# Optimization experiments

Measured on AMD Instinct MI355X. Metric: run time of the kernel, lower is better.

The kernel has to match this reference:

```python
import jax, jax.numpy as jnp
import numpy as np

B = 256; NROIS = 200; IN = 200; HID = 128; L = 4; H = 8; RATIO = 0.5
K = int(np.ceil(RATIO * NROIS))        # SAGPooling top-k per graph = 100
N = B * NROIS                          # total nodes = 51200
DEG = 32; EPG = NROIS * DEG; E_EDGES = B * EPG  # 1,638,400 edges
EMB = HID * L                          # MHA embed dim = 512
DH = EMB // H

def _xavier(k, shape):
    fan_in, fan_out = shape[-2], shape[-1]
    lim = float(np.sqrt(6.0 / (fan_in + fan_out)))
    return jax.random.uniform(k, shape, jnp.float32, -lim, lim)

def setup_inputs() -> dict:
    key = jax.random.key(0)
    ks = jax.random.split(key, 16)
    x = jax.random.normal(ks[0], (N, IN), jnp.float32)
    # block-diagonal edge list: edges stay within each graph's node range
    src = jax.random.randint(ks[1], (E_EDGES,), 0, NROIS, jnp.int32)
    dst = jax.random.randint(ks[2], (E_EDGES,), 0, NROIS, jnp.int32)
    off = jnp.repeat(jnp.arange(B, dtype=jnp.int32) * NROIS, EPG)
    edge_index = jnp.stack([src + off, dst + off])
    edge_attr = jax.random.normal(ks[3], (E_EDGES,), jnp.float32)  # unused by the math
    batch = jnp.repeat(jnp.arange(B, dtype=jnp.int32), NROIS)
    return dict(
        x=x, edge_index=edge_index, edge_attr=edge_attr, batch=batch,
        gcn_w0=_xavier(ks[4], (IN, HID)),
        gcn_w=_xavier(ks[5], (L - 1, HID, HID)),
        gcn_b=jnp.zeros((L, HID), jnp.float32),
        lin1_w0=_xavier(ks[6], (IN + HID, HID)),
        lin1_w=_xavier(ks[7], (L - 1, 2 * HID, HID)),
        lin1_b=jnp.zeros((L, HID), jnp.float32),
        lin2_w=_xavier(ks[8], (L, HID, HID)),
        lin2_b=jnp.zeros((L, HID), jnp.float32),
        sag_w1=_xavier(ks[9], (HID, 1)),
        sag_w2=_xavier(ks[10], (HID, 1)),
        sag_b=jnp.zeros((1,), jnp.float32),
        mha_in_w=_xavier(ks[11], (3 * EMB, EMB)),
        mha_in_b=jnp.zeros((3 * EMB,), jnp.float32),
        mha_out_w=_xavier(ks[12], (EMB, EMB)),
        mha_out_b=jnp.zeros((EMB,), jnp.float32),
        fin_w=_xavier(ks[13], (EMB, HID)),
        fin_b=jnp.zeros((HID,), jnp.float32),
    )

def _gcn_conv(x, src, dst, W, b):
    xw = x @ W
    deg = jax.ops.segment_sum(jnp.ones_like(dst, jnp.float32), dst, num_segments=N) + 1.0
    dinv = jax.lax.rsqrt(deg)
    norm = dinv[src] * dinv[dst]                     # [E]
    agg = jax.ops.segment_sum(xw[src] * norm[:, None], dst, num_segments=N)
    agg = agg + xw * (dinv * dinv)[:, None]          # self-loop term
    return agg + b

def _gcblock(x, src, dst, gw, gb, l1w, l1b, l2w, l2b):
    x1 = jnp.tanh(_gcn_conv(x, src, dst, gw, gb))
    h = jnp.tanh(jnp.concatenate([x, x1], axis=1) @ l1w + l1b)
    return jnp.tanh(h @ l2w + l2b)

def _sag_pool_pad(z, src, dst, w1, w2, b):
    # SAGPooling score via PyG GraphConv (aggr='add'): lin_rel(sum_j x_j) + lin_root(x_i)
    neigh = jax.ops.segment_sum(z[src], dst, num_segments=N)
    score = (neigh @ w1)[:, 0] + b[0] + (z @ w2)[:, 0]        # [N]
    s3 = score.reshape(B, NROIS)
    vals, idx = jax.lax.top_k(s3, K)                           # [B,K]
    z3 = z.reshape(B, NROIS, HID)
    pooled = jnp.take_along_axis(z3, idx[:, :, None], axis=1) * jnp.tanh(vals)[:, :, None]
    zpad = jnp.zeros_like(z3).at[jnp.arange(B)[:, None], idx].set(pooled)
    return zpad.reshape(N, HID)

def reference(x, edge_index, edge_attr, batch,
              gcn_w0, gcn_w, gcn_b, lin1_w0, lin1_w, lin1_b, lin2_w, lin2_b,
              sag_w1, sag_w2, sag_b,
              mha_in_w, mha_in_b, mha_out_w, mha_out_b, fin_w, fin_b):
    src, dst = edge_index[0], edge_index[1]
    z = x
    pads = []
    for i in range(L):
        gw = gcn_w0 if i == 0 else gcn_w[i - 1]
        l1w = lin1_w0 if i == 0 else lin1_w[i - 1]
        z = _gcblock(z, src, dst, gw, gcn_b[i], l1w, lin1_b[i], lin2_w[i], lin2_b[i])
        pads.append(_sag_pool_pad(z, src, dst, sag_w1, sag_w2, sag_b))
    xc = jnp.concatenate(pads, axis=1).reshape(B, NROIS, EMB)   # [B,S,E]
    # MultiheadAttention (batch_first, eval mode -> no dropout)
    qkv = xc @ mha_in_w.T + mha_in_b                             # [B,S,3E]
    q, k, v = jnp.split(qkv, 3, axis=-1)
    def heads(t):
        return t.reshape(B, NROIS, H, DH).transpose(0, 2, 1, 3)  # [B,H,S,dh]
    q, k, v = heads(q), heads(k), heads(v)
    scores = jnp.einsum('bhqd,bhkd->bhqk', q, k) / np.sqrt(DH)
    attn = jax.nn.softmax(scores, axis=-1)                       # [B,H,S,S]
    o = jnp.einsum('bhqk,bhkd->bhqd', attn, v).transpose(0, 2, 1, 3).reshape(B, NROIS, EMB)
    o = o @ mha_out_w.T + mha_out_b
    attn_weights = attn.mean(axis=1)                             # avg over heads [B,S,S]
    # readout: global_mean_pool over each graph's nrois nodes
    pooled = o.mean(axis=1)                                      # [B,E]
    out = jnp.tanh(pooled @ fin_w + fin_b)                       # [B,HID]
    return out, attn_weights
```

## Files before the change

kernel.cpp:

```cpp
#include <hip/hip_runtime.h>
#include <hip/hip_fp16.h>


#define GB   256
#define SS   200
#define KIN  200
#define HD   128
#define NLAY 4
#define NHD  8
#define TOPK 100
#define NT   (GB * SS)
#define EPG_ 6400
#define NE_  (GB * EPG_)
#define EMB_ 512

typedef _Float16 half8 __attribute__((ext_vector_type(8)));
typedef _Float16 half4v __attribute__((ext_vector_type(4)));
typedef float floatx4 __attribute__((ext_vector_type(4)));

__global__ __launch_bounds__(256) void k_build_A(const int* __restrict__ src,
                                                 const int* __restrict__ dst,
                                                 float* __restrict__ A) {
  int e = blockIdx.x * 256 + threadIdx.x;
  if (e >= NE_) return;
  int d = dst[e], s = src[e];
  int b = d / SS;
  int dl = d - b * SS;
  int sl = s - b * SS;
  atomicAdd(&A[((size_t)b * SS + dl) * SS + sl], 1.0f);
}

__global__ __launch_bounds__(256) void k_dinv(const float* __restrict__ A,
                                              float* __restrict__ dinv) {
  int node = blockIdx.x * 4 + (threadIdx.x >> 6);
  int lane = threadIdx.x & 63;
  const float* r = A + (size_t)node * SS;
  float v = r[lane] + r[lane + 64] + r[lane + 128];
  if (lane < 8) v += r[lane + 192];
#pragma unroll
  for (int o = 32; o; o >>= 1) v += __shfl_xor(v, o);
  if (lane == 0) dinv[node] = rsqrtf(v + 1.0f);
}

__global__ __launch_bounds__(256) void k_prep_all(
    const float* __restrict__ gcn_w0, const float* __restrict__ gcn_w,
    const float* __restrict__ lin1_w0, const float* __restrict__ lin1_w,
    const float* __restrict__ lin2_w,
    __half* __restrict__ whi, __half* __restrict__ wlo) {
  const int mat = blockIdx.x >> 7;
  const int n   = blockIdx.x & 127;
  const int l = mat / 3, which = mat % 3;
  const float* src;
  int K, Kpad;
  if (which == 0) {
    K = l ? HD : KIN;  Kpad = l ? 128 : 256;
    src = l ? gcn_w + (size_t)(l - 1) * HD * HD : gcn_w0;
  } else if (which == 1) {
    K = l ? 2 * HD : KIN + HD;  Kpad = l ? 256 : 384;
    src = l ? lin1_w + (size_t)(l - 1) * 2 * HD * HD : lin1_w0;
  } else {
    K = HD;  Kpad = HD;
    src = lin2_w + (size_t)l * HD * HD;
  }
  int off = (l == 0) ? (which == 0 ? 0 : (which == 1 ? 32768 : 81920))
                     : 98304 + (l - 1) * 65536 +
                       (which == 0 ? 0 : (which == 1 ? 16384 : 49152));
  _Float16* wh = (_Float16*)whi + (size_t)off + (size_t)n * Kpad;
  _Float16* wl = (_Float16*)wlo + (size_t)off + (size_t)n * Kpad;
  for (int k = threadIdx.x; k < Kpad; k += 256) {
    float v = (k < K) ? src[(size_t)k * HD + n] : 0.f;
    _Float16 h = (_Float16)v;
    wh[k] = h;
    wl[k] = (_Float16)(v - (float)h);
  }
}

__global__ __launch_bounds__(256) void k_prep_w16(const float* __restrict__ W,
                                                  __half* __restrict__ W16) {
  int i = blockIdx.x * 256 + threadIdx.x;
  float4 v = reinterpret_cast<const float4*>(W)[i];
  half4v h = {(_Float16)v.x, (_Float16)v.y, (_Float16)v.z, (_Float16)v.w};
  *reinterpret_cast<half4v*>((_Float16*)W16 + (size_t)i * 4) = h;
}

__global__ __launch_bounds__(256) void k_node_mfma(
    const float* __restrict__ in1, int k1,
    const float* __restrict__ in2,
    const __half* __restrict__ Whi, const __half* __restrict__ Wlo,
    int Kpad,
    const float* __restrict__ bias,
    float* __restrict__ out, int doTanh) {
  const int m0 = blockIdx.x * 64;
  const int t = threadIdx.x;
  const int wave = t >> 6, lane = t & 63;
  const int col = lane & 15, quad = lane >> 4;
  const int wm = (wave & 1) * 32;
  const int wn = (wave >> 1) * 64;
  __shared__ __align__(16) _Float16 Ah[64][72];
  __shared__ __align__(16) _Float16 Al[64][72];
  floatx4 acc[2][4] = {};
  const int lr = t >> 2;
  const int lk = (t & 3) * 16;
  const _Float16* Wh = (const _Float16*)Whi;
  const _Float16* Wl = (const _Float16*)Wlo;

  for (int k0 = 0; k0 < Kpad; k0 += 64) {
    __syncthreads();
#pragma unroll
    for (int q = 0; q < 4; ++q) {
      int kg = k0 + lk + q * 4;
      float4 v = {0.f, 0.f, 0.f, 0.f};
      if (kg < k1)
        v = *reinterpret_cast<const float4*>(&in1[(size_t)(m0 + lr) * k1 + kg]);
      else if (in2 && kg < k1 + HD)
        v = *reinterpret_cast<const float4*>(&in2[(size_t)(m0 + lr) * HD + (kg - k1)]);
      half4v h = {(_Float16)v.x, (_Float16)v.y, (_Float16)v.z, (_Float16)v.w};
      half4v lo = {(_Float16)(v.x - (float)h.x), (_Float16)(v.y - (float)h.y),
                   (_Float16)(v.z - (float)h.z), (_Float16)(v.w - (float)h.w)};
      *reinterpret_cast<half4v*>(&Ah[lr][lk + q * 4]) = h;
      *reinterpret_cast<half4v*>(&Al[lr][lk + q * 4]) = lo;
    }
    __syncthreads();
#pragma unroll
    for (int ks = 0; ks < 2; ++ks) {
      half8 ah[2], al[2], bh[4], bl[4];
#pragma unroll
      for (int i = 0; i < 2; ++i) {
        ah[i] = *reinterpret_cast<const half8*>(&Ah[wm + i * 16 + col][ks * 32 + quad * 8]);
        al[i] = *reinterpret_cast<const half8*>(&Al[wm + i * 16 + col][ks * 32 + quad * 8]);
      }
#pragma unroll
      for (int j = 0; j < 4; ++j) {
        const size_t wo = (size_t)(wn + j * 16 + col) * Kpad + k0 + ks * 32 + quad * 8;
        bh[j] = *reinterpret_cast<const half8*>(Wh + wo);
        bl[j] = *reinterpret_cast<const half8*>(Wl + wo);
      }
#pragma unroll
      for (int i = 0; i < 2; ++i)
#pragma unroll
        for (int j = 0; j < 4; ++j) {
          acc[i][j] = __builtin_amdgcn_mfma_f32_16x16x32_f16(ah[i], bh[j], acc[i][j], 0, 0, 0);
          acc[i][j] = __builtin_amdgcn_mfma_f32_16x16x32_f16(ah[i], bl[j], acc[i][j], 0, 0, 0);
          acc[i][j] = __builtin_amdgcn_mfma_f32_16x16x32_f16(al[i], bh[j], acc[i][j], 0, 0, 0);
        }
    }
  }
#pragma unroll
  for (int j = 0; j < 4; ++j) {
    int n = wn + j * 16 + col;
    float bb = bias ? bias[n] : 0.f;
#pragma unroll
    for (int i = 0; i < 2; ++i) {
      int rbase = m0 + wm + i * 16 + quad * 4;
#pragma unroll
      for (int r = 0; r < 4; ++r) {
        float v = acc[i][j][r] + bb;
        if (doTanh) v = tanhf(v);
        out[(size_t)(rbase + r) * HD + n] = v;
      }
    }
  }
}

__global__ __launch_bounds__(256) void k_fused(
    const float* __restrict__ in1, int k1,
    const float* __restrict__ x1,
    const __half* __restrict__ l1wh, const __half* __restrict__ l1wl, int KP1,
    const float* __restrict__ l1b,
    const __half* __restrict__ l2wh, const __half* __restrict__ l2wl,
    const float* __restrict__ l2b,
    const __half* __restrict__ gwh, const __half* __restrict__ gwl,
    float* __restrict__ zout, float* __restrict__ xwout) {
  const int m0 = blockIdx.x * 64;
  const int t = threadIdx.x;
  const int wave = t >> 6, lane = t & 63;
  const int col = lane & 15, quad = lane >> 4;
  const int wm = (wave & 1) * 32;
  const int wn = (wave >> 1) * 64;
  __shared__ __align__(16) _Float16 Ah[64][72];
  __shared__ __align__(16) _Float16 Al[64][72];
  __shared__ __align__(16) _Float16 Hh[64][136];
  __shared__ __align__(16) _Float16 Hl[64][136];
  const int lr = t >> 2;
  const int lk = (t & 3) * 16;

  {
    floatx4 acc[2][4] = {};
    for (int k0 = 0; k0 < KP1; k0 += 64) {
      __syncthreads();
#pragma unroll
      for (int q = 0; q < 4; ++q) {
        int kg = k0 + lk + q * 4;
        float4 v = {0.f, 0.f, 0.f, 0.f};
        if (kg < k1)
          v = *reinterpret_cast<const float4*>(&in1[(size_t)(m0 + lr) * k1 + kg]);
        else if (kg < k1 + HD)
          v = *reinterpret_cast<const float4*>(&x1[(size_t)(m0 + lr) * HD + (kg - k1)]);
        half4v h = {(_Float16)v.x, (_Float16)v.y, (_Float16)v.z, (_Float16)v.w};
        half4v lo = {(_Float16)(v.x - (float)h.x), (_Float16)(v.y - (float)h.y),
                     (_Float16)(v.z - (float)h.z), (_Float16)(v.w - (float)h.w)};
        *reinterpret_cast<half4v*>(&Ah[lr][lk + q * 4]) = h;
        *reinterpret_cast<half4v*>(&Al[lr][lk + q * 4]) = lo;
      }
      __syncthreads();
#pragma unroll
      for (int ks = 0; ks < 2; ++ks) {
        half8 ah[2], al[2], bh[4], bl[4];
#pragma unroll
        for (int i = 0; i < 2; ++i) {
          ah[i] = *reinterpret_cast<const half8*>(&Ah[wm + i * 16 + col][ks * 32 + quad * 8]);
          al[i] = *reinterpret_cast<const half8*>(&Al[wm + i * 16 + col][ks * 32 + quad * 8]);
        }
#pragma unroll
        for (int j = 0; j < 4; ++j) {
          const size_t wo = (size_t)(wn + j * 16 + col) * KP1 + k0 + ks * 32 + quad * 8;
          bh[j] = *reinterpret_cast<const half8*>((const _Float16*)l1wh + wo);
          bl[j] = *reinterpret_cast<const half8*>((const _Float16*)l1wl + wo);
        }
#pragma unroll
        for (int i = 0; i < 2; ++i)
#pragma unroll
          for (int j = 0; j < 4; ++j) {
            acc[i][j] = __builtin_amdgcn_mfma_f32_16x16x32_f16(ah[i], bh[j], acc[i][j], 0, 0, 0);
            acc[i][j] = __builtin_amdgcn_mfma_f32_16x16x32_f16(ah[i], bl[j], acc[i][j], 0, 0, 0);
            acc[i][j] = __builtin_amdgcn_mfma_f32_16x16x32_f16(al[i], bh[j], acc[i][j], 0, 0, 0);
          }
      }
    }
#pragma unroll
    for (int j = 0; j < 4; ++j) {
      int n = wn + j * 16 + col;
      float bb = l1b[n];
#pragma unroll
      for (int i = 0; i < 2; ++i) {
        int rb = wm + i * 16 + quad * 4;
#pragma unroll
        for (int r = 0; r < 4; ++r) {
          float v = tanhf(acc[i][j][r] + bb);
          _Float16 h = (_Float16)v;
          Hh[rb + r][n] = h;
          Hl[rb + r][n] = (_Float16)(v - (float)h);
        }
      }
    }
  }
  __syncthreads();

  {
    floatx4 acc[2][4] = {};
#pragma unroll
    for (int kc = 0; kc < 4; ++kc) {
      half8 ah[2], al[2], bh[4], bl[4];
#pragma unroll
      for (int i = 0; i < 2; ++i) {
        ah[i] = *reinterpret_cast<const half8*>(&Hh[wm + i * 16 + col][kc * 32 + quad * 8]);
        al[i] = *reinterpret_cast<const half8*>(&Hl[wm + i * 16 + col][kc * 32 + quad * 8]);
      }
#pragma unroll
      for (int j = 0; j < 4; ++j) {
        const size_t wo = (size_t)(wn + j * 16 + col) * HD + kc * 32 + quad * 8;
        bh[j] = *reinterpret_cast<const half8*>((const _Float16*)l2wh + wo);
        bl[j] = *reinterpret_cast<const half8*>((const _Float16*)l2wl + wo);
      }
#pragma unroll
      for (int i = 0; i < 2; ++i)
#pragma unroll
        for (int j = 0; j < 4; ++j) {
          acc[i][j] = __builtin_amdgcn_mfma_f32_16x16x32_f16(ah[i], bh[j], acc[i][j], 0, 0, 0);
          acc[i][j] = __builtin_amdgcn_mfma_f32_16x16x32_f16(ah[i], bl[j], acc[i][j], 0, 0, 0);
          acc[i][j] = __builtin_amdgcn_mfma_f32_16x16x32_f16(al[i], bh[j], acc[i][j], 0, 0, 0);
        }
    }
    __syncthreads();
#pragma unroll
    for (int j = 0; j < 4; ++j) {
      int n = wn + j * 16 + col;
      float bb = l2b[n];
#pragma unroll
      for (int i = 0; i < 2; ++i) {
        int rb = wm + i * 16 + quad * 4;
#pragma unroll
        for (int r = 0; r < 4; ++r) {
          float v = tanhf(acc[i][j][r] + bb);
          zout[(size_t)(m0 + rb + r) * HD + n] = v;
          _Float16 h = (_Float16)v;
          Hh[rb + r][n] = h;
          Hl[rb + r][n] = (_Float16)(v - (float)h);
        }
      }
    }
  }
  if (!gwh) return;
  __syncthreads();

  {
    floatx4 acc[2][4] = {};
#pragma unroll
    for (int kc = 0; kc < 4; ++kc) {
      half8 ah[2], al[2], bh[4], bl[4];
#pragma unroll
      for (int i = 0; i < 2; ++i) {
        ah[i] = *reinterpret_cast<const half8*>(&Hh[wm + i * 16 + col][kc * 32 + quad * 8]);
        al[i] = *reinterpret_cast<const half8*>(&Hl[wm + i * 16 + col][kc * 32 + quad * 8]);
      }
#pragma unroll
      for (int j = 0; j < 4; ++j) {
        const size_t wo = (size_t)(wn + j * 16 + col) * HD + kc * 32 + quad * 8;
        bh[j] = *reinterpret_cast<const half8*>((const _Float16*)gwh + wo);
        bl[j] = *reinterpret_cast<const half8*>((const _Float16*)gwl + wo);
      }
#pragma unroll
      for (int i = 0; i < 2; ++i)
#pragma unroll
        for (int j = 0; j < 4; ++j) {
          acc[i][j] = __builtin_amdgcn_mfma_f32_16x16x32_f16(ah[i], bh[j], acc[i][j], 0, 0, 0);
          acc[i][j] = __builtin_amdgcn_mfma_f32_16x16x32_f16(ah[i], bl[j], acc[i][j], 0, 0, 0);
          acc[i][j] = __builtin_amdgcn_mfma_f32_16x16x32_f16(al[i], bh[j], acc[i][j], 0, 0, 0);
        }
    }
#pragma unroll
    for (int j = 0; j < 4; ++j) {
      int n = wn + j * 16 + col;
#pragma unroll
      for (int i = 0; i < 2; ++i) {
        int rb = wm + i * 16 + quad * 4;
#pragma unroll
        for (int r = 0; r < 4; ++r)
          xwout[(size_t)(m0 + rb + r) * HD + n] = acc[i][j][r];
      }
    }
  }
}

__global__ __launch_bounds__(256) void k_agg_mfma(
    const float* __restrict__ A, const float* __restrict__ dinv,
    const float* __restrict__ xw, const float* __restrict__ bias,
    float* __restrict__ out) {
  const int b    = blockIdx.x >> 1;
  const int row0 = (blockIdx.x & 1) * 128;
  const int t = threadIdx.x;
  const int wave = t >> 6, lane = t & 63;
  const int col = lane & 15, quad = lane >> 4;
  const int wm = (wave & 1) * 64, wn = (wave >> 1) * 64;
  __shared__ __align__(16) _Float16 Ah[128][72];
  __shared__ __align__(16) _Float16 Al[128][72];
  __shared__ __align__(16) _Float16 Bh[128][72];
  __shared__ __align__(16) _Float16 Bl[128][72];
  __shared__ float dvs[256];
  dvs[t] = (t < SS) ? dinv[b * SS + t] : 0.f;
  floatx4 acc[4][4] = {};
  const float* Ab  = A  + (size_t)b * SS * SS;
  const float* xwb = xw + (size_t)b * SS * HD;
  const int lr = t >> 1, lk = (t & 1) * 32;
  const int d = row0 + lr;
  __syncthreads();
  const float dvd = (d < SS) ? dvs[d] : 0.f;

  for (int k0 = 0; k0 < 256; k0 += 64) {
    __syncthreads();
#pragma unroll
    for (int q = 0; q < 8; ++q) {
      int s = k0 + lk + q * 4;
      float4 v = {0.f, 0.f, 0.f, 0.f};
      if (d < SS && s < SS)
        v = *reinterpret_cast<const float4*>(&Ab[(size_t)d * SS + s]);
      float e0 = (v.x + ((s + 0 == d) ? 1.f : 0.f)) * dvd * dvs[(s + 0) & 255];
      float e1 = (v.y + ((s + 1 == d) ? 1.f : 0.f)) * dvd * dvs[(s + 1) & 255];
      float e2 = (v.z + ((s + 2 == d) ? 1.f : 0.f)) * dvd * dvs[(s + 2) & 255];
      float e3 = (v.w + ((s + 3 == d) ? 1.f : 0.f)) * dvd * dvs[(s + 3) & 255];
      half4v h = {(_Float16)e0, (_Float16)e1, (_Float16)e2, (_Float16)e3};
      half4v lo = {(_Float16)(e0 - (float)h.x), (_Float16)(e1 - (float)h.y),
                   (_Float16)(e2 - (float)h.z), (_Float16)(e3 - (float)h.w)};
      *reinterpret_cast<half4v*>(&Ah[lr][lk + q * 4]) = h;
      *reinterpret_cast<half4v*>(&Al[lr][lk + q * 4]) = lo;
    }
#pragma unroll
    for (int p = 0; p < 8; ++p) {
      int idx = t + p * 256;
      int c4 = idx & 31, ss = idx >> 5;
      int s = k0 + ss;
      float4 v = {0.f, 0.f, 0.f, 0.f};
      if (s < SS)
        v = *reinterpret_cast<const float4*>(&xwb[(size_t)s * HD + c4 * 4]);
      int ssx = ss ^ ((c4 & 7) << 3);
      float e[4] = {v.x, v.y, v.z, v.w};
#pragma unroll
      for (int j = 0; j < 4; ++j) {
        _Float16 h = (_Float16)e[j];
        Bh[c4 * 4 + j][ssx] = h;
        Bl[c4 * 4 + j][ssx] = (_Float16)(e[j] - (float)h);
      }
    }
    __syncthreads();
#pragma unroll
    for (int ks = 0; ks < 2; ++ks) {
      half8 ah[4], al[4], bh[4], bl[4];
#pragma unroll
      for (int i = 0; i < 4; ++i) {
        ah[i] = *reinterpret_cast<const half8*>(&Ah[wm + i * 16 + col][ks * 32 + quad * 8]);
        al[i] = *reinterpret_cast<const half8*>(&Al[wm + i * 16 + col][ks * 32 + quad * 8]);
      }
#pragma unroll
      for (int j = 0; j < 4; ++j) {
        int n = wn + j * 16 + col;
        int koff = (ks * 32 + quad * 8) ^ (((n >> 2) & 7) << 3);
        bh[j] = *reinterpret_cast<const half8*>(&Bh[n][koff]);
        bl[j] = *reinterpret_cast<const half8*>(&Bl[n][koff]);
      }
#pragma unroll
      for (int i = 0; i < 4; ++i)
#pragma unroll
        for (int j = 0; j < 4; ++j) {
          acc[i][j] = __builtin_amdgcn_mfma_f32_16x16x32_f16(ah[i], bh[j], acc[i][j], 0, 0, 0);
          acc[i][j] = __builtin_amdgcn_mfma_f32_16x16x32_f16(ah[i], bl[j], acc[i][j], 0, 0, 0);
          acc[i][j] = __builtin_amdgcn_mfma_f32_16x16x32_f16(al[i], bh[j], acc[i][j], 0, 0, 0);
        }
    }
  }
#pragma unroll
  for (int j = 0; j < 4; ++j) {
    int n = wn + j * 16 + col;
    float bb = bias[n];
#pragma unroll
    for (int i = 0; i < 4; ++i) {
      int rbase = row0 + wm + i * 16 + quad * 4;
#pragma unroll
      for (int r = 0; r < 4; ++r) {
        int row = rbase + r;
        if (row < SS)
          out[((size_t)b * SS + row) * HD + n] = tanhf(acc[i][j][r] + bb);
      }
    }
  }
}

__global__ __launch_bounds__(256) void k_sag(
    const float* __restrict__ z, const float* __restrict__ A,
    const float* __restrict__ w1, const float* __restrict__ w2,
    const float* __restrict__ sb,
    __half* __restrict__ xch, __half* __restrict__ xcl, int layer) {
  const int b = blockIdx.x, t = threadIdx.x;
  __shared__ float w1s[HD], w2s[HD];
  __shared__ float zw1[SS], sc[SS], fac[SS];
  if (t < HD) { w1s[t] = w1[t]; w2s[t] = w2[t]; }
  __syncthreads();
  float a2 = 0.f;
  if (t < SS) {
    const float4* zr = reinterpret_cast<const float4*>(&z[((size_t)b * SS + t) * HD]);
    float a1 = 0.f;
#pragma unroll
    for (int q = 0; q < HD / 4; ++q) {
      float4 v = zr[q];
      a1 += v.x * w1s[4 * q] + v.y * w1s[4 * q + 1] + v.z * w1s[4 * q + 2] + v.w * w1s[4 * q + 3];
      a2 += v.x * w2s[4 * q] + v.y * w2s[4 * q + 1] + v.z * w2s[4 * q + 2] + v.w * w2s[4 * q + 3];
    }
    zw1[t] = a1;
  }
  __syncthreads();
  if (t < SS) {
    float s = sb[0] + a2;
    const float4* ar = reinterpret_cast<const float4*>(&A[((size_t)b * SS + t) * SS]);
#pragma unroll 5
    for (int q = 0; q < SS / 4; ++q) {
      float4 v = ar[q];
      s += v.x * zw1[4 * q] + v.y * zw1[4 * q + 1] + v.z * zw1[4 * q + 2] + v.w * zw1[4 * q + 3];
    }
    sc[t] = s;
  }
  __syncthreads();
  if (t < SS) {
    float si = sc[t];
    int cnt = 0;
    for (int j = 0; j < SS; ++j) {
      float sj = sc[j];
      cnt += (sj > si || (sj == si && j < t)) ? 1 : 0;
    }
    fac[t] = (cnt < TOPK) ? tanhf(si) : 0.f;
  }
  __syncthreads();
  _Float16* xh = (_Float16*)xch;
  _Float16* xl = (_Float16*)xcl;
  for (int idx = t; idx < SS * HD; idx += 256) {
    int row = idx >> 7, c = idx & 127;
    float v = fac[row] * z[((size_t)b * SS + row) * HD + c];
    _Float16 h = (_Float16)v;
    size_t o = ((size_t)b * SS + row) * EMB_ + layer * HD + c;
    xh[o] = h;
    xl[o] = (_Float16)(v - (float)h);
  }
}

__global__ __launch_bounds__(256) void k_proj(
    const __half* __restrict__ xch, const __half* __restrict__ Win16,
    const float* __restrict__ bin, __half* __restrict__ QKh) {
  const int wg = (blockIdx.x & 7) * 400 + (blockIdx.x >> 3);
  const int bm = wg >> 3;
  const int bn = wg & 7;
  const int m0 = bm * 128, n0 = bn * 128;
  const int t = threadIdx.x;
  const int wave = t >> 6, lane = t & 63;
  const int col = lane & 15, quad = lane >> 4;
  const int wm = (wave & 1) * 64;
  const int wn = (wave >> 1) * 64;
  __shared__ __align__(16) _Float16 As[128][64];
  __shared__ __align__(16) _Float16 Bs[128][64];
  floatx4 acc[4][4] = {};
  const _Float16* X = (const _Float16*)xch;
  const _Float16* W = (const _Float16*)Win16;

  const int srow = lane >> 3;
  const int sch  = (lane & 7) ^ srow;
  const int arow = wave * 8 + srow;
  const int fsw = col & 7;

  for (int k0 = 0; k0 < EMB_; k0 += 64) {
#pragma unroll
    for (int q = 0; q < 4; ++q) {
      const _Float16* ga = X + (size_t)(m0 + q * 32 + arow) * EMB_ + k0 + sch * 8;
      __builtin_amdgcn_global_load_lds(
          (const __attribute__((address_space(1))) void*)ga,
          (__attribute__((address_space(3))) void*)((char*)&As[0][0] + q * 4096 + wave * 1024),
          16, 0, 0);
      const _Float16* gb = W + (size_t)(n0 + q * 32 + arow) * EMB_ + k0 + sch * 8;
      __builtin_amdgcn_global_load_lds(
          (const __attribute__((address_space(1))) void*)gb,
          (__attribute__((address_space(3))) void*)((char*)&Bs[0][0] + q * 4096 + wave * 1024),
          16, 0, 0);
    }
    __syncthreads();
#pragma unroll
    for (int ks = 0; ks < 2; ++ks) {
      const int ch = (ks * 4 + quad) ^ fsw;
      half8 af[4], bf[4];
#pragma unroll
      for (int i = 0; i < 4; ++i)
        af[i] = *reinterpret_cast<const half8*>(
            (const char*)&As[0][0] + (wm + i * 16 + col) * 128 + ch * 16);
#pragma unroll
      for (int j = 0; j < 4; ++j)
        bf[j] = *reinterpret_cast<const half8*>(
            (const char*)&Bs[0][0] + (wn + j * 16 + col) * 128 + ch * 16);
#pragma unroll
      for (int i = 0; i < 4; ++i)
#pragma unroll
        for (int j = 0; j < 4; ++j)
          acc[i][j] = __builtin_amdgcn_mfma_f32_16x16x32_f16(af[i], bf[j], acc[i][j], 0, 0, 0);
    }
    __syncthreads();
  }
#pragma unroll
  for (int j = 0; j < 4; ++j) {
    int c = n0 + wn + j * 16 + col;
    float bb = bin[c];
#pragma unroll
    for (int i = 0; i < 4; ++i) {
      int rbase = m0 + wm + i * 16 + quad * 4;
#pragma unroll
      for (int r = 0; r < 4; ++r)
        QKh[(size_t)(rbase + r) * 1024 + c] = __float2half(acc[i][j][r] + bb);
    }
  }
}

__global__ __launch_bounds__(256) void k_attn(
    const __half* __restrict__ QKh,
    float* __restrict__ cpbuf,
    float* __restrict__ attn) {
  const int bx = (blockIdx.x & 7) * 416 + (blockIdx.x >> 3);
  const int b  = bx / 13;
  const int it = bx % 13;
  const int i0 = it * 16;
  const int rows = (SS - i0 >= 16) ? 16 : (SS - i0);
  const int t    = threadIdx.x;
  const int wave = t >> 6;
  const int lane = t & 63;
  const int col  = lane & 15;
  const int quad = lane >> 4;

  __shared__ __align__(16) float Ss[16][212];

  float am[13];
  int   soff[13];
  int   kmax = 0;
#pragma unroll
  for (int k = 0; k < 13; ++k) {
    int idx = t + (k << 8);
    am[k] = 0.f;
    if (idx < rows * 200) {
      int i = idx / 200;
      soff[k] = idx + 12 * i;
      kmax = k + 1;
    } else soff[k] = 0;
  }

  const _Float16* Qbase = (const _Float16*)QKh + (size_t)b * SS * 1024;
  const _Float16* qrow = Qbase + (size_t)(i0 + col) * 1024 + quad * 8;
  const _Float16* krow[4];
#pragma unroll
  for (int m = 0; m < 4; ++m) {
    int jt = wave + m * 4;
    krow[m] = Qbase + (size_t)(jt * 16 + col) * 1024 + 512 + quad * 8;
  }

  for (int h = 0; h < NHD; ++h) {
    const int hoff = h * 64;
    half8 a0 = *reinterpret_cast<const half8*>(qrow + hoff);
    half8 a1 = *reinterpret_cast<const half8*>(qrow + hoff + 32);
#pragma unroll
    for (int m = 0; m < 4; ++m) {
      int jt = wave + m * 4;
      if (jt < 13) {
        half8 b0 = *reinterpret_cast<const half8*>(krow[m] + hoff);
        half8 b1 = *reinterpret_cast<const half8*>(krow[m] + hoff + 32);
        floatx4 acc = {0.f, 0.f, 0.f, 0.f};
        acc = __builtin_amdgcn_mfma_f32_16x16x32_f16(a0, b0, acc, 0, 0, 0);
        acc = __builtin_amdgcn_mfma_f32_16x16x32_f16(a1, b1, acc, 0, 0, 0);
#pragma unroll
        for (int r = 0; r < 4; ++r)
          Ss[quad * 4 + r][jt * 16 + col] = acc[r] * 0.125f;
      }
    }
    __syncthreads();
#pragma unroll
    for (int ri = 0; ri < 4; ++ri) {
      int r = wave * 4 + ri;
      if (r < rows) {
        float* srow = &Ss[r][0];
        float s0 = srow[lane], s1 = srow[lane + 64], s2 = srow[lane + 128];
        float s3 = (lane < 8) ? srow[lane + 192] : -1e30f;
        float mx = fmaxf(fmaxf(s0, s1), fmaxf(s2, s3));
#pragma unroll
        for (int o = 32; o; o >>= 1) mx = fmaxf(mx, __shfl_xor(mx, o));
        float e0 = __expf(s0 - mx), e1 = __expf(s1 - mx), e2 = __expf(s2 - mx);
        float e3 = (lane < 8) ? __expf(s3 - mx) : 0.f;
        float sum = e0 + e1 + e2 + e3;
#pragma unroll
        for (int o = 32; o; o >>= 1) sum += __shfl_xor(sum, o);
        float rl = 1.0f / sum;
        srow[lane] = e0 * rl; srow[lane + 64] = e1 * rl; srow[lane + 128] = e2 * rl;
        if (lane < 8) srow[lane + 192] = e3 * rl;
      }
    }
    __syncthreads();
    const float* sflat = &Ss[0][0];
#pragma unroll
    for (int k = 0; k < 13; ++k)
      if (k < kmax) am[k] += sflat[soff[k]] * 0.125f;
    if (t < SS) {
      float s = 0.f;
      for (int i = 0; i < rows; ++i) s += Ss[i][t];
      atomicAdd(&cpbuf[((size_t)b * NHD + h) * SS + t], s);
    }
    __syncthreads();
  }
  float* abase = &attn[((size_t)b * SS + i0) * SS];
#pragma unroll
  for (int k = 0; k < 13; ++k)
    if (k < kmax) abase[t + (k << 8)] = am[k];
}

__global__ __launch_bounds__(256) void k_pool(
    const __half* __restrict__ xch, const __half* __restrict__ xcl,
    const float* __restrict__ cpbuf,
    const float* __restrict__ Win, const float* __restrict__ bin,
    float* __restrict__ pooled) {
  const int b = blockIdx.x, t = threadIdx.x;
  __shared__ float cps[NHD][SS];
  __shared__ float tvs[NHD][EMB_];
  for (int idx = t; idx < NHD * SS; idx += 256) {
    int h = idx / SS, j = idx - h * SS;
    cps[h][j] = cpbuf[((size_t)b * NHD + h) * SS + j];
  }
  __syncthreads();
  const _Float16* xh = (const _Float16*)xch + (size_t)b * SS * EMB_;
  const _Float16* xl = (const _Float16*)xcl + (size_t)b * SS * EMB_;
  float a0[NHD] = {0.f}, a1[NHD] = {0.f};
  for (int j = 0; j < SS; ++j) {
    float x0 = (float)xh[(size_t)j * EMB_ + t] + (float)xl[(size_t)j * EMB_ + t];
    float x1 = (float)xh[(size_t)j * EMB_ + t + 256] + (float)xl[(size_t)j * EMB_ + t + 256];
#pragma unroll
    for (int h = 0; h < NHD; ++h) {
      float c = cps[h][j];
      a0[h] += c * x0; a1[h] += c * x1;
    }
  }
#pragma unroll
  for (int h = 0; h < NHD; ++h) { tvs[h][t] = a0[h]; tvs[h][t + 256] = a1[h]; }
  __syncthreads();
  const int wv = t >> 6, lane = t & 63;
  for (int e = wv; e < EMB_; e += 4) {
    int h = e >> 6;
    const float* wr = Win + (size_t)(2 * EMB_ + e) * EMB_;
    float s = 0.f;
#pragma unroll
    for (int q = 0; q < 8; ++q) s += wr[lane + q * 64] * tvs[h][lane + q * 64];
#pragma unroll
    for (int o = 32; o; o >>= 1) s += __shfl_xor(s, o);
    if (lane == 0) pooled[(size_t)b * EMB_ + e] = bin[2 * EMB_ + e] * (float)SS + s;
  }
}

__global__ __launch_bounds__(256) void k_final(
    const float* __restrict__ pooled, const float* __restrict__ Wout,
    const float* __restrict__ bout, const float* __restrict__ finw,
    const float* __restrict__ finb, float* __restrict__ out) {
  const int b = blockIdx.x, t = threadIdx.x;
  __shared__ float pl[EMB_], po[EMB_];
  for (int k = t; k < EMB_; k += 256) pl[k] = pooled[(size_t)b * EMB_ + k] * (1.0f / (float)SS);
  __syncthreads();
  for (int e = t; e < EMB_; e += 256) {
    const float* wr = &Wout[(size_t)e * EMB_];
    float a = bout[e];
    for (int k = 0; k < EMB_; ++k) a += wr[k] * pl[k];
    po[e] = a;
  }
  __syncthreads();
  if (t < HD) {
    float a = finb[t];
    for (int e = 0; e < EMB_; ++e) a += po[e] * finw[(size_t)e * HD + t];
    out[(size_t)b * HD + t] = tanhf(a);
  }
}

extern "C" void kernel_launch(void* const* d_in, const int* in_sizes, int n_in,
                              void* d_out, int out_size, void* d_ws, size_t ws_size,
                              hipStream_t stream) {
  const float* x         = (const float*)d_in[0];
  const int*   ei        = (const int*)d_in[1];
  const float* gcn_w0    = (const float*)d_in[4];
  const float* gcn_w     = (const float*)d_in[5];
  const float* gcn_b     = (const float*)d_in[6];
  const float* lin1_w0   = (const float*)d_in[7];
  const float* lin1_w    = (const float*)d_in[8];
  const float* lin1_b    = (const float*)d_in[9];
  const float* lin2_w    = (const float*)d_in[10];
  const float* lin2_b    = (const float*)d_in[11];
  const float* sag_w1    = (const float*)d_in[12];
  const float* sag_w2    = (const float*)d_in[13];
  const float* sag_b     = (const float*)d_in[14];
  const float* mha_in_w  = (const float*)d_in[15];
  const float* mha_in_b  = (const float*)d_in[16];
  const float* mha_out_w = (const float*)d_in[17];
  const float* mha_out_b = (const float*)d_in[18];
  const float* fin_w     = (const float*)d_in[19];
  const float* fin_b     = (const float*)d_in[20];

  float* ws     = (float*)d_ws;
  float* dinv   = ws;
  float* Araw   = dinv + NT;
  float* buf0   = Araw + (size_t)GB * SS * SS;
  float* buf1   = buf0 + (size_t)NT * HD;
  float* zbuf   = buf1 + (size_t)NT * HD;
  float* xcf    = zbuf + (size_t)NT * HD;
  __half* xch   = (__half*)xcf;
  __half* xcl   = xch + (size_t)NT * EMB_;
  float* pooled = xcf + (size_t)NT * EMB_;
  __half* QKh  = (__half*)Araw;
  float* cpbuf = Araw + 26214400;

  float* outp = (float*)d_out;
  float* attn = outp + (size_t)GB * HD;

  __half* whi   = (__half*)attn;
  __half* wlo   = whi + 294912;
  __half* Win16 = wlo + 294912;

  hipMemsetAsync(Araw, 0, (size_t)GB * SS * SS * sizeof(float), stream);

  k_prep_all<<<12 * 128, 256, 0, stream>>>(gcn_w0, gcn_w, lin1_w0, lin1_w, lin2_w, whi, wlo);
  k_prep_w16<<<512, 256, 0, stream>>>(mha_in_w, Win16);
  k_build_A<<<NE_ / 256, 256, 0, stream>>>(ei, ei + NE_, Araw);
  k_dinv<<<NT / 4, 256, 0, stream>>>(Araw, dinv);

  static const int KP1[4]  = {384, 256, 256, 256};
  static const int OFFg[4] = {0, 98304, 163840, 229376};
  static const int OFF1[4] = {32768, 114688, 180224, 245760};
  static const int OFF2[4] = {81920, 147456, 212992, 278528};

  k_node_mfma<<<NT / 64, 256, 0, stream>>>(x, KIN, nullptr,
                                           whi + OFFg[0], wlo + OFFg[0], 256,
                                           nullptr, buf0, 0);

  for (int l = 0; l < NLAY; ++l) {
    const float* zin = (l == 0) ? x : zbuf;
    int k1 = (l == 0) ? KIN : HD;
    k_agg_mfma<<<GB * 2, 256, 0, stream>>>(Araw, dinv, buf0, gcn_b + l * HD, buf1);
    k_fused<<<NT / 64, 256, 0, stream>>>(
        zin, k1, buf1,
        whi + OFF1[l], wlo + OFF1[l], KP1[l], lin1_b + l * HD,
        whi + OFF2[l], wlo + OFF2[l], lin2_b + l * HD,
        (l < NLAY - 1) ? whi + OFFg[l + 1] : (const __half*)nullptr,
        (l < NLAY - 1) ? wlo + OFFg[l + 1] : (const __half*)nullptr,
        zbuf, buf0);
    k_sag<<<GB, 256, 0, stream>>>(zbuf, Araw, sag_w1, sag_w2, sag_b, xch, xcl, l);
  }

  hipMemsetAsync(cpbuf, 0, (size_t)GB * NHD * SS * sizeof(float), stream);
  k_proj<<<(NT / 128) * 8, 256, 0, stream>>>(xch, Win16, mha_in_b, QKh);
  k_attn<<<GB * 13, 256, 0, stream>>>(QKh, cpbuf, attn);
  k_pool<<<GB, 256, 0, stream>>>(xch, xcl, cpbuf, mha_in_w, mha_in_b, pooled);
  k_final<<<GB, 256, 0, stream>>>(pooled, mha_out_w, mha_out_b, fin_w, fin_b, outp);
}
```

Baseline: 1.372 ms.

## Factor GCN normalization out of A, drop A-lo MFMA, retile softmax and SAG dot

In the GCN aggregation, the D^-1/2 scaling moves off the adjacency tile. Source-side scaling goes onto the xw operand and destination-side scaling onto the epilogue, so A+I (small integer counts) fits exactly in fp16. That removes the low-half A buffer and one of three MFMAs per tile. The SAG score loop gets four independent accumulators, and the attention softmax switches from one row per wave to sixteen lanes per row, using shorter shuffles across all 256 threads. The A split is exact only while edge counts stay fp16-representable.

```diff
diff --git a/kernel.cpp b/kernel.cpp
--- a/kernel.cpp
+++ b/kernel.cpp
@@ -343,7 +343,6 @@
   const int col = lane & 15, quad = lane >> 4;
   const int wm = (wave & 1) * 64, wn = (wave >> 1) * 64;
   __shared__ __align__(16) _Float16 Ah[128][72];
-  __shared__ __align__(16) _Float16 Al[128][72];
   __shared__ __align__(16) _Float16 Bh[128][72];
   __shared__ __align__(16) _Float16 Bl[128][72];
   __shared__ float dvs[256];
@@ -354,7 +353,6 @@
   const int lr = t >> 1, lk = (t & 1) * 32;
   const int d = row0 + lr;
   __syncthreads();
-  const float dvd = (d < SS) ? dvs[d] : 0.f;
 
   for (int k0 = 0; k0 < 256; k0 += 64) {
     __syncthreads();
@@ -364,15 +362,12 @@
       float4 v = {0.f, 0.f, 0.f, 0.f};
       if (d < SS && s < SS)
         v = *reinterpret_cast<const float4*>(&Ab[(size_t)d * SS + s]);
-      float e0 = (v.x + ((s + 0 == d) ? 1.f : 0.f)) * dvd * dvs[(s + 0) & 255];
-      float e1 = (v.y + ((s + 1 == d) ? 1.f : 0.f)) * dvd * dvs[(s + 1) & 255];
-      float e2 = (v.z + ((s + 2 == d) ? 1.f : 0.f)) * dvd * dvs[(s + 2) & 255];
-      float e3 = (v.w + ((s + 3 == d) ? 1.f : 0.f)) * dvd * dvs[(s + 3) & 255];
-      half4v h = {(_Float16)e0, (_Float16)e1, (_Float16)e2, (_Float16)e3};
-      half4v lo = {(_Float16)(e0 - (float)h.x), (_Float16)(e1 - (float)h.y),
-                   (_Float16)(e2 - (float)h.z), (_Float16)(e3 - (float)h.w)};
+      if (s + 0 == d) v.x += 1.0f;
+      if (s + 1 == d) v.y += 1.0f;
+      if (s + 2 == d) v.z += 1.0f;
+      if (s + 3 == d) v.w += 1.0f;
+      half4v h = {(_Float16)v.x, (_Float16)v.y, (_Float16)v.z, (_Float16)v.w};
       *reinterpret_cast<half4v*>(&Ah[lr][lk + q * 4]) = h;
-      *reinterpret_cast<half4v*>(&Al[lr][lk + q * 4]) = lo;
     }
 #pragma unroll
     for (int p = 0; p < 8; ++p) {
@@ -382,8 +377,9 @@
       float4 v = {0.f, 0.f, 0.f, 0.f};
       if (s < SS)
         v = *reinterpret_cast<const float4*>(&xwb[(size_t)s * HD + c4 * 4]);
+      float dvv = dvs[s & 255];
       int ssx = ss ^ ((c4 & 7) << 3);
-      float e[4] = {v.x, v.y, v.z, v.w};
+      float e[4] = {v.x * dvv, v.y * dvv, v.z * dvv, v.w * dvv};
 #pragma unroll
       for (int j = 0; j < 4; ++j) {
         _Float16 h = (_Float16)e[j];
@@ -394,12 +390,10 @@
     __syncthreads();
 #pragma unroll
     for (int ks = 0; ks < 2; ++ks) {
-      half8 ah[4], al[4], bh[4], bl[4];
-#pragma unroll
-      for (int i = 0; i < 4; ++i) {
+      half8 ah[4], bh[4], bl[4];
+#pragma unroll
+      for (int i = 0; i < 4; ++i)
         ah[i] = *reinterpret_cast<const half8*>(&Ah[wm + i * 16 + col][ks * 32 + quad * 8]);
-        al[i] = *reinterpret_cast<const half8*>(&Al[wm + i * 16 + col][ks * 32 + quad * 8]);
-      }
 #pragma unroll
       for (int j = 0; j < 4; ++j) {
         int n = wn + j * 16 + col;
@@ -413,7 +407,6 @@
         for (int j = 0; j < 4; ++j) {
           acc[i][j] = __builtin_amdgcn_mfma_f32_16x16x32_f16(ah[i], bh[j], acc[i][j], 0, 0, 0);
           acc[i][j] = __builtin_amdgcn_mfma_f32_16x16x32_f16(ah[i], bl[j], acc[i][j], 0, 0, 0);
-          acc[i][j] = __builtin_amdgcn_mfma_f32_16x16x32_f16(al[i], bh[j], acc[i][j], 0, 0, 0);
         }
     }
   }
@@ -428,7 +421,7 @@
       for (int r = 0; r < 4; ++r) {
         int row = rbase + r;
         if (row < SS)
-          out[((size_t)b * SS + row) * HD + n] = tanhf(acc[i][j][r] + bb);
+          out[((size_t)b * SS + row) * HD + n] = tanhf(dvs[row] * acc[i][j][r] + bb);
       }
     }
   }
@@ -458,14 +451,21 @@
   }
   __syncthreads();
   if (t < SS) {
-    float s = sb[0] + a2;
+    float s0 = 0.f, s1 = 0.f, s2 = 0.f, s3 = 0.f;
     const float4* ar = reinterpret_cast<const float4*>(&A[((size_t)b * SS + t) * SS]);
-#pragma unroll 5
-    for (int q = 0; q < SS / 4; ++q) {
-      float4 v = ar[q];
-      s += v.x * zw1[4 * q] + v.y * zw1[4 * q + 1] + v.z * zw1[4 * q + 2] + v.w * zw1[4 * q + 3];
-    }
-    sc[t] = s;
+#pragma unroll
+    for (int q = 0; q < SS / 4; q += 4) {
+      float4 v0 = ar[q], v1 = ar[q + 1];
+      float4 v2 = (q + 2 < SS / 4) ? ar[q + 2] : float4{0.f, 0.f, 0.f, 0.f};
+      float4 v3 = (q + 3 < SS / 4) ? ar[q + 3] : float4{0.f, 0.f, 0.f, 0.f};
+      s0 += v0.x * zw1[4 * q] + v0.y * zw1[4 * q + 1] + v0.z * zw1[4 * q + 2] + v0.w * zw1[4 * q + 3];
+      s1 += v1.x * zw1[4 * q + 4] + v1.y * zw1[4 * q + 5] + v1.z * zw1[4 * q + 6] + v1.w * zw1[4 * q + 7];
+      if (q + 2 < SS / 4)
+        s2 += v2.x * zw1[4 * q + 8] + v2.y * zw1[4 * q + 9] + v2.z * zw1[4 * q + 10] + v2.w * zw1[4 * q + 11];
+      if (q + 3 < SS / 4)
+        s3 += v3.x * zw1[4 * q + 12] + v3.y * zw1[4 * q + 13] + v3.z * zw1[4 * q + 14] + v3.w * zw1[4 * q + 15];
+    }
+    sc[t] = sb[0] + a2 + ((s0 + s1) + (s2 + s3));
   }
   __syncthreads();
   if (t < SS) {
@@ -576,6 +576,8 @@
   const int lane = t & 63;
   const int col  = lane & 15;
   const int quad = lane >> 4;
+  const int srow_ = t >> 4;
+  const int ssub_ = t & 15;
 
   __shared__ __align__(16) float Ss[16][212];
 
@@ -621,24 +623,30 @@
       }
     }
     __syncthreads();
-#pragma unroll
-    for (int ri = 0; ri < 4; ++ri) {
-      int r = wave * 4 + ri;
-      if (r < rows) {
-        float* srow = &Ss[r][0];
-        float s0 = srow[lane], s1 = srow[lane + 64], s2 = srow[lane + 128];
-        float s3 = (lane < 8) ? srow[lane + 192] : -1e30f;
-        float mx = fmaxf(fmaxf(s0, s1), fmaxf(s2, s3));
-#pragma unroll
-        for (int o = 32; o; o >>= 1) mx = fmaxf(mx, __shfl_xor(mx, o));
-        float e0 = __expf(s0 - mx), e1 = __expf(s1 - mx), e2 = __expf(s2 - mx);
-        float e3 = (lane < 8) ? __expf(s3 - mx) : 0.f;
-        float sum = e0 + e1 + e2 + e3;
-#pragma unroll
-        for (int o = 32; o; o >>= 1) sum += __shfl_xor(sum, o);
-        float rl = 1.0f / sum;
-        srow[lane] = e0 * rl; srow[lane + 64] = e1 * rl; srow[lane + 128] = e2 * rl;
-        if (lane < 8) srow[lane + 192] = e3 * rl;
+    if (srow_ < rows) {
+      float v[13];
+      float mx = -1e30f;
+#pragma unroll
+      for (int i2 = 0; i2 < 13; ++i2) {
+        int c = ssub_ + i2 * 16;
+        v[i2] = (c < 200) ? Ss[srow_][c] : -1e30f;
+        mx = fmaxf(mx, v[i2]);
+      }
+#pragma unroll
+      for (int m = 8; m; m >>= 1) mx = fmaxf(mx, __shfl_xor(mx, m));
+      float sum = 0.f;
+#pragma unroll
+      for (int i2 = 0; i2 < 13; ++i2) {
+        v[i2] = __expf(v[i2] - mx);
+        sum += v[i2];
+      }
+#pragma unroll
+      for (int m = 8; m; m >>= 1) sum += __shfl_xor(sum, m);
+      float rl = 1.0f / sum;
+#pragma unroll
+      for (int i2 = 0; i2 < 13; ++i2) {
+        int c = ssub_ + i2 * 16;
+        if (c < 200) Ss[srow_][c] = v[i2] * rl;
       }
     }
     __syncthreads();
```

Result: slower. 1.411 ms (+2.8%).
